# Optimization experiments

Measured on AMD Instinct MI355X. Metric: run time of the kernel, lower is better.

The kernel has to match this reference:

```python
import jax, jax.numpy as jnp
import numpy as np
from jax import lax

WS = 8           # window size
NH = 16          # num heads
BN_EPS = 1e-5


def _rel_pos_index(ws):
    # static Swin relative-position index, shape (ws*ws, ws*ws)
    coords = jnp.stack(jnp.meshgrid(jnp.arange(ws), jnp.arange(ws), indexing='ij'))  # (2,ws,ws)
    cf = coords.reshape(2, -1)                                   # (2, n)
    rel = cf[:, :, None] - cf[:, None, :]                        # (2, n, n)
    return (rel[0] + ws - 1) * (2 * ws - 1) + (rel[1] + ws - 1)  # (n, n)


def setup_inputs() -> dict:
    key = jax.random.key(0)
    ks = jax.random.split(key, 9)
    C = 256
    x = jax.random.normal(ks[0], (2, C, 256, 256), dtype=jnp.float32)
    qkv_w = jax.random.normal(ks[1], (3 * C, C), dtype=jnp.float32) * 0.02
    bias_table = jax.random.normal(ks[2], ((2 * WS - 1) ** 2, NH), dtype=jnp.float32) * 0.02
    dw_w = jax.random.normal(ks[3], (C, 1, 3, 3), dtype=jnp.float32) * 0.1
    bn_gamma = 1.0 + 0.1 * jax.random.normal(ks[4], (C,), dtype=jnp.float32)
    bn_beta = 0.1 * jax.random.normal(ks[5], (C,), dtype=jnp.float32)
    bn_mean = 0.1 * jax.random.normal(ks[6], (C,), dtype=jnp.float32)
    bn_var = jax.random.uniform(ks[7], (C,), dtype=jnp.float32) + 0.5
    pw_w = jax.random.normal(ks[8], (C, C), dtype=jnp.float32) * 0.05
    return {"x": x, "qkv_w": qkv_w, "bias_table": bias_table, "dw_w": dw_w,
            "bn_gamma": bn_gamma, "bn_beta": bn_beta, "bn_mean": bn_mean,
            "bn_var": bn_var, "pw_w": pw_w}


def _lmsa(x, qkv_w, bias_table, dw_w, bn_gamma, bn_beta, bn_mean, bn_var, pw_w):
    B, C, H, W = x.shape
    h, ws = NH, WS
    d = C // h
    scale = d ** (-0.5)
    short = x
    # pad H,W to multiples of ws (reflect); static no-op if already divisible
    pad_h, pad_w = (-H) % ws, (-W) % ws
    if pad_h or pad_w:
        x = jnp.pad(x, ((0, 0), (0, 0), (0, pad_h), (0, pad_w)), mode='reflect')
    Hp, Wp = x.shape[2], x.shape[3]
    hh, ww = Hp // ws, Wp // ws
    # 1x1 conv qkv: C -> 3C
    qkv = jnp.einsum('oc,bchw->bohw', qkv_w, x)
    # window partition: (B,3C,Hp,Wp) -> (3, B*hh*ww, h, ws*ws, d)
    qkv = qkv.reshape(B, 3, h, d, hh, ws, ww, ws)
    qkv = qkv.transpose(1, 0, 4, 6, 2, 5, 7, 3).reshape(3, B * hh * ww, h, ws * ws, d)
    q, k, v = qkv[0], qkv[1], qkv[2]
    dots = jnp.einsum('bhid,bhjd->bhij', q, k) * scale
    # relative position bias
    idx = _rel_pos_index(ws)                       # (n, n)
    bias = bias_table[idx]                         # (n, n, h)
    dots = dots + bias.transpose(2, 0, 1)[None]    # (1, h, n, n)
    attn = jax.nn.softmax(dots, axis=-1)
    out = jnp.einsum('bhij,bhjd->bhid', attn, v)
    # window merge: -> (B, C, Hp, Wp)
    out = out.reshape(B, hh, ww, h, ws, ws, d).transpose(0, 3, 6, 1, 4, 2, 5)
    out = out.reshape(B, C, Hp, Wp)
    out = out[:, :, :H, :W] + short
    # pad_out: reflect pad right/bottom by 1
    out = jnp.pad(out, ((0, 0), (0, 0), (0, 1), (0, 1)), mode='reflect')
    # proj = SeparableConvBN: depthwise3x3 -> BN (inference) -> pointwise1x1
    y = lax.conv_general_dilated(out, dw_w, window_strides=(1, 1),
                                 padding=((1, 1), (1, 1)),
                                 feature_group_count=C,
                                 dimension_numbers=('NCHW', 'OIHW', 'NCHW'))
    inv = bn_gamma / jnp.sqrt(bn_var + BN_EPS)
    y = y * inv[None, :, None, None] + (bn_beta - bn_mean * inv)[None, :, None, None]
    y = jnp.einsum('oc,bchw->bohw', pw_w, y)
    return y[:, :, :H, :W]


def reference(x, qkv_w, bias_table, dw_w, bn_gamma, bn_beta, bn_mean, bn_var, pw_w):
    return _lmsa(x, qkv_w, bias_table, dw_w, bn_gamma, bn_beta, bn_mean, bn_var, pw_w)
```

## Files before the change

kernel.cpp:

```cpp
#include <hip/hip_runtime.h>
#include <hip/hip_bf16.h>

typedef unsigned short us;
typedef unsigned int   u32;
typedef __bf16 bf16_t;
typedef bf16_t bf16x8 __attribute__((ext_vector_type(8)));
typedef float  f32x4  __attribute__((ext_vector_type(4)));
typedef us     usx4   __attribute__((ext_vector_type(4)));
typedef us     usx8   __attribute__((ext_vector_type(8)));

#define HWSZ 65536

__device__ __forceinline__ float b2f(us u) {
    union { u32 i; float f; } t; t.i = ((u32)u) << 16; return t.f;
}
__device__ __forceinline__ us f2b(float f) {
    union { float f; u32 i; } t; t.f = f;
    u32 r = t.i + 0x7fff + ((t.i >> 16) & 1);
    return (us)(r >> 16);
}
__device__ __forceinline__ void gl_lds16(const us* g, us* l) {
    __builtin_amdgcn_global_load_lds(
        (const __attribute__((address_space(1))) u32*)g,
        (__attribute__((address_space(3))) u32*)l, 16, 0, 0);
}

__global__ __launch_bounds__(256) void prep(
        const float* __restrict__ qkv_w, const float* __restrict__ pw_w,
        const float* __restrict__ g, const float* __restrict__ bt,
        const float* __restrict__ mn, const float* __restrict__ vr,
        us* __restrict__ wb, us* __restrict__ pwb, float* __restrict__ ivad) {
    int tid = blockIdx.x * 256 + threadIdx.x;
    if (tid < 768 * 256) wb[tid] = f2b(qkv_w[tid]);
    if (tid < 256 * 256) pwb[tid] = f2b(pw_w[tid]);
    if (tid < 256) {
        float iv = g[tid] / sqrtf(vr[tid] + 1e-5f);
        ivad[tid] = iv;
        ivad[256 + tid] = bt[tid] - mn[tid] * iv;
    }
}

__global__ __launch_bounds__(256) void transpose_x(
        const float* __restrict__ x, us* __restrict__ xt) {
    __shared__ float ls[64][65];
    const int b  = blockIdx.z;
    const int c0 = blockIdx.y * 64;
    const int p0 = blockIdx.x * 64;
    const int tid = threadIdx.x;
    const int tr  = tid >> 4;
    const int tc4 = (tid & 15) << 2;
    const float* xb = x + ((size_t)b * 256 + c0) * HWSZ + p0;
    #pragma unroll
    for (int q = 0; q < 4; ++q) {
        int c = tr + 16 * q;
        float4 v = *(const float4*)&xb[(size_t)c * HWSZ + tc4];
        ls[c][tc4 + 0] = v.x; ls[c][tc4 + 1] = v.y;
        ls[c][tc4 + 2] = v.z; ls[c][tc4 + 3] = v.w;
    }
    __syncthreads();
    #pragma unroll
    for (int q = 0; q < 4; ++q) {
        int pp = tr + 16 * q;
        usx4 o;
        o[0] = f2b(ls[tc4 + 0][pp]); o[1] = f2b(ls[tc4 + 1][pp]);
        o[2] = f2b(ls[tc4 + 2][pp]); o[3] = f2b(ls[tc4 + 3][pp]);
        *(usx4*)&xt[((size_t)b * HWSZ + p0 + pp) * 256 + c0 + tc4] = o;
    }
}

__global__ __launch_bounds__(256) void qkv_mfma(
        const us* __restrict__ xt, const us* __restrict__ wb,
        us* __restrict__ qkv) {
    __shared__ __align__(16) us As[128 * 32];
    __shared__ __align__(16) us Bs[128 * 32];
    const int tid  = threadIdx.x;
    const int wv   = tid >> 6;
    const int lane = tid & 63;
    const int p0 = blockIdx.x * 128;
    const int o0 = blockIdx.y * 128;
    const int b  = blockIdx.z;
    const us* Ab = xt + ((size_t)b * HWSZ + p0) * 256;
    const us* Bb = wb + (size_t)o0 * 256;
    const int lr = lane & 15;
    const int k8 = lane >> 4;
    const int wm = wv >> 1, wn = wv & 1;
    const int srow = lane >> 2;
    const int sch  = (lane & 3) << 3;

    f32x4 acc[4][4];
    #pragma unroll
    for (int i = 0; i < 4; ++i)
        #pragma unroll
        for (int j = 0; j < 4; ++j) acc[i][j] = (f32x4){0.f, 0.f, 0.f, 0.f};

    for (int kt = 0; kt < 8; ++kt) {
        const int c0 = kt * 32;
        #pragma unroll
        for (int i = 0; i < 2; ++i) {
            int rb = 32 * wv + 16 * i;
            gl_lds16(Ab + (size_t)(rb + srow) * 256 + c0 + sch, &As[rb * 32]);
            gl_lds16(Bb + (size_t)(rb + srow) * 256 + c0 + sch, &Bs[rb * 32]);
        }
        __syncthreads();
        bf16x8 af[4], bg[4];
        #pragma unroll
        for (int i = 0; i < 4; ++i)
            af[i] = *(const bf16x8*)&As[(64 * wm + 16 * i + lr) * 32 + k8 * 8];
        #pragma unroll
        for (int j = 0; j < 4; ++j)
            bg[j] = *(const bf16x8*)&Bs[(64 * wn + 16 * j + lr) * 32 + k8 * 8];
        #pragma unroll
        for (int i = 0; i < 4; ++i)
            #pragma unroll
            for (int j = 0; j < 4; ++j)
                acc[i][j] = __builtin_amdgcn_mfma_f32_16x16x32_bf16(
                    af[i], bg[j], acc[i][j], 0, 0, 0);
        __syncthreads();
    }
    #pragma unroll
    for (int i = 0; i < 4; ++i) {
        int pr = p0 + 64 * wm + 16 * i + 4 * k8;
        #pragma unroll
        for (int j = 0; j < 4; ++j) {
            int oc = o0 + 64 * wn + 16 * j + lr;
            #pragma unroll
            for (int rr = 0; rr < 4; ++rr)
                qkv[((size_t)b * HWSZ + pr + rr) * 768 + oc] = f2b(acc[i][j][rr]);
        }
    }
}

__global__ __launch_bounds__(64) void attn_kernel(
        const us* __restrict__ qkv, const us* __restrict__ xt,
        const float* __restrict__ bias_table, us* __restrict__ att) {
    const int bx = blockIdx.x;
    const int head = bx & 15;
    const int w = (bx >> 4) & 1023;
    const int b = bx >> 14;
    const int wy = w >> 5, wx = w & 31;
    const int t = threadIdx.x;
    const int p = (wy * 8 + (t >> 3)) * 256 + wx * 8 + (t & 7);
    const size_t rowb = (size_t)b * HWSZ + p;
    const size_t gq = rowb * 768 + head * 16;

    __shared__ float ks[64][20];
    __shared__ float vs[64][20];
    __shared__ float bias_s[228];

    usx8 k0v = *(const usx8*)&qkv[gq + 256];
    usx8 k1v = *(const usx8*)&qkv[gq + 256 + 8];
    usx8 v0v = *(const usx8*)&qkv[gq + 512];
    usx8 v1v = *(const usx8*)&qkv[gq + 512 + 8];
    #pragma unroll
    for (int d = 0; d < 8; ++d) {
        ks[t][d] = b2f(k0v[d]); ks[t][d + 8] = b2f(k1v[d]);
        vs[t][d] = b2f(v0v[d]); vs[t][d + 8] = b2f(v1v[d]);
    }
    usx8 q0 = *(const usx8*)&qkv[gq];
    usx8 q1 = *(const usx8*)&qkv[gq + 8];
    float qr[16];
    #pragma unroll
    for (int d = 0; d < 8; ++d) {
        qr[d] = b2f(q0[d]) * 0.25f; qr[d + 8] = b2f(q1[d]) * 0.25f;
    }
    #pragma unroll
    for (int r = 0; r < 4; ++r) {
        int idx = r * 64 + t;
        if (idx < 225) bias_s[idx] = bias_table[idx * 16 + head];
    }
    __syncthreads();

    float dots[64];
    #pragma unroll 16
    for (int j = 0; j < 64; ++j) {
        float kk[16];
        *(float4*)&kk[0]  = *(const float4*)&ks[j][0];
        *(float4*)&kk[4]  = *(const float4*)&ks[j][4];
        *(float4*)&kk[8]  = *(const float4*)&ks[j][8];
        *(float4*)&kk[12] = *(const float4*)&ks[j][12];
        float s = 0.f;
        #pragma unroll
        for (int d = 0; d < 16; ++d) s = fmaf(qr[d], kk[d], s);
        dots[j] = s;
    }
    const int iy = t >> 3, ix = t & 7;
    float mx = -1e30f;
    #pragma unroll
    for (int j = 0; j < 64; ++j) {
        int jy = j >> 3, jx = j & 7;
        dots[j] += bias_s[(iy - jy + 7) * 15 + (ix - jx + 7)];
        mx = fmaxf(mx, dots[j]);
    }
    float ssum = 0.f;
    #pragma unroll
    for (int j = 0; j < 64; ++j) {
        float e = __expf(dots[j] - mx);
        dots[j] = e; ssum += e;
    }
    const float sinv = 1.0f / ssum;

    float o[16];
    #pragma unroll
    for (int d = 0; d < 16; ++d) o[d] = 0.f;
    #pragma unroll 16
    for (int j = 0; j < 64; ++j) {
        float vv[16];
        *(float4*)&vv[0]  = *(const float4*)&vs[j][0];
        *(float4*)&vv[4]  = *(const float4*)&vs[j][4];
        *(float4*)&vv[8]  = *(const float4*)&vs[j][8];
        *(float4*)&vv[12] = *(const float4*)&vs[j][12];
        float a = dots[j];
        #pragma unroll
        for (int d = 0; d < 16; ++d) o[d] = fmaf(a, vv[d], o[d]);
    }
    usx8 r0 = *(const usx8*)&xt[rowb * 256 + head * 16];
    usx8 r1 = *(const usx8*)&xt[rowb * 256 + head * 16 + 8];
    usx8 s0, s1;
    #pragma unroll
    for (int d = 0; d < 8; ++d) {
        s0[d] = f2b(o[d] * sinv + b2f(r0[d]));
        s1[d] = f2b(o[d + 8] * sinv + b2f(r1[d]));
    }
    *(usx8*)&att[rowb * 256 + head * 16]     = s0;
    *(usx8*)&att[rowb * 256 + head * 16 + 8] = s1;
}

__global__ __launch_bounds__(256) void dwbn(
        const us* __restrict__ att, const float* __restrict__ dw_w,
        const float* __restrict__ ivad, us* __restrict__ ybn) {
    const int tid = threadIdx.x;
    const int cg = tid & 63;
    const int pl = tid >> 6;
    const int b  = blockIdx.y;
    const int pbase = blockIdx.x * 256;
    const int c4 = cg * 4;
    float w[9][4], iv[4], ad[4];
    #pragma unroll
    for (int cc = 0; cc < 4; ++cc) {
        #pragma unroll
        for (int k = 0; k < 9; ++k) w[k][cc] = dw_w[(c4 + cc) * 9 + k];
        iv[cc] = ivad[c4 + cc];
        ad[cc] = ivad[256 + c4 + cc];
    }
    const us* ab = att + (size_t)b * HWSZ * 256;
    us* yb = ybn + (size_t)b * HWSZ * 256;
    for (int ch = 0; ch < 64; ++ch) {
        const int p = pbase + ch * 4 + pl;
        const int y = p >> 8, x = p & 255;
        float acc[4] = {0.f, 0.f, 0.f, 0.f};
        #pragma unroll
        for (int dy = -1; dy <= 1; ++dy) {
            int yy = y + dy;
            if (yy < 0) continue;
            if (yy > 255) yy = 254;
            #pragma unroll
            for (int dx = -1; dx <= 1; ++dx) {
                int xx = x + dx;
                if (xx < 0) continue;
                if (xx > 255) xx = 254;
                usx4 vv = *(const usx4*)&ab[((size_t)(yy << 8) + xx) * 256 + c4];
                const int k = (dy + 1) * 3 + dx + 1;
                acc[0] = fmaf(w[k][0], b2f(vv[0]), acc[0]);
                acc[1] = fmaf(w[k][1], b2f(vv[1]), acc[1]);
                acc[2] = fmaf(w[k][2], b2f(vv[2]), acc[2]);
                acc[3] = fmaf(w[k][3], b2f(vv[3]), acc[3]);
            }
        }
        usx4 o;
        o[0] = f2b(acc[0] * iv[0] + ad[0]);
        o[1] = f2b(acc[1] * iv[1] + ad[1]);
        o[2] = f2b(acc[2] * iv[2] + ad[2]);
        o[3] = f2b(acc[3] * iv[3] + ad[3]);
        *(usx4*)&yb[(size_t)p * 256 + c4] = o;
    }
}

__global__ __launch_bounds__(256) void pw_mfma(
        const us* __restrict__ ybn, const us* __restrict__ pwb,
        float* __restrict__ out) {
    __shared__ __align__(16) us As[128 * 32];
    __shared__ __align__(16) us Bs[128 * 32];
    const int tid  = threadIdx.x;
    const int wv   = tid >> 6;
    const int lane = tid & 63;
    const int p0 = blockIdx.x * 128;
    const int o0 = blockIdx.y * 128;
    const int b  = blockIdx.z;
    const us* Ab = ybn + ((size_t)b * HWSZ + p0) * 256;
    const us* Bb = pwb + (size_t)o0 * 256;
    const int lr = lane & 15;
    const int k8 = lane >> 4;
    const int wm = wv >> 1, wn = wv & 1;
    const int srow = lane >> 2;
    const int sch  = (lane & 3) << 3;

    f32x4 acc[4][4];
    #pragma unroll
    for (int i = 0; i < 4; ++i)
        #pragma unroll
        for (int j = 0; j < 4; ++j) acc[i][j] = (f32x4){0.f, 0.f, 0.f, 0.f};

    for (int kt = 0; kt < 8; ++kt) {
        const int c0 = kt * 32;
        #pragma unroll
        for (int i = 0; i < 2; ++i) {
            int rb = 32 * wv + 16 * i;
            gl_lds16(Ab + (size_t)(rb + srow) * 256 + c0 + sch, &As[rb * 32]);
            gl_lds16(Bb + (size_t)(rb + srow) * 256 + c0 + sch, &Bs[rb * 32]);
        }
        __syncthreads();
        bf16x8 af[4], bg[4];
        #pragma unroll
        for (int i = 0; i < 4; ++i)
            af[i] = *(const bf16x8*)&As[(64 * wm + 16 * i + lr) * 32 + k8 * 8];
        #pragma unroll
        for (int j = 0; j < 4; ++j)
            bg[j] = *(const bf16x8*)&Bs[(64 * wn + 16 * j + lr) * 32 + k8 * 8];
        #pragma unroll
        for (int i = 0; i < 4; ++i)
            #pragma unroll
            for (int j = 0; j < 4; ++j)
                acc[i][j] = __builtin_amdgcn_mfma_f32_16x16x32_bf16(
                    af[i], bg[j], acc[i][j], 0, 0, 0);
        __syncthreads();
    }
    #pragma unroll
    for (int i = 0; i < 4; ++i) {
        int pr = p0 + 64 * wm + 16 * i + 4 * k8;
        #pragma unroll
        for (int j = 0; j < 4; ++j) {
            int oc = o0 + 64 * wn + 16 * j + lr;
            *(f32x4*)&out[((size_t)b * 256 + oc) * HWSZ + pr] = acc[i][j];
        }
    }
}

extern "C" void kernel_launch(void* const* d_in, const int* in_sizes, int n_in,
                              void* d_out, int out_size, void* d_ws, size_t ws_size,
                              hipStream_t stream) {
    const float* x          = (const float*)d_in[0];
    const float* qkv_w      = (const float*)d_in[1];
    const float* bias_table = (const float*)d_in[2];
    const float* dw_w       = (const float*)d_in[3];
    const float* bn_gamma   = (const float*)d_in[4];
    const float* bn_beta    = (const float*)d_in[5];
    const float* bn_mean    = (const float*)d_in[6];
    const float* bn_var     = (const float*)d_in[7];
    const float* pw_w       = (const float*)d_in[8];
    float* out = (float*)d_out;

    char* ws = (char*)d_ws;
    us*    xt   = (us*)ws;
    us*    qkv  = (us*)(ws + 67108864);
    us*    att  = (us*)(ws + 268435456);
    us*    wb   = (us*)(ws + 335544320);
    us*    pwb  = (us*)(ws + 335937536);
    float* ivad = (float*)(ws + 336068608);
    us*    ybn  = xt;

    prep<<<768, 256, 0, stream>>>(qkv_w, pw_w, bn_gamma, bn_beta, bn_mean,
                                  bn_var, wb, pwb, ivad);
    transpose_x<<<dim3(1024, 4, 2), 256, 0, stream>>>(x, xt);
    qkv_mfma<<<dim3(512, 6, 2), 256, 0, stream>>>(xt, wb, qkv);
    attn_kernel<<<2 * 1024 * 16, 64, 0, stream>>>(qkv, xt, bias_table, att);
    dwbn<<<dim3(256, 2), 256, 0, stream>>>(att, dw_w, ivad, ybn);
    pw_mfma<<<dim3(512, 2, 2), 256, 0, stream>>>(ybn, pwb, out);
}
```

Baseline: 1.131 ms.

## Restructure attention per window, vectorize qkv stores and depthwise conv loads

Attention now runs one 256-thread block per window that handles all 16 heads, staging K/V for eight heads at a time in LDS as bf16 via direct global-to-LDS loads, replacing 64-thread per-head blocks. The q scale is folded into the qkv weights during prep. The qkv GEMM swaps its MFMA operands so each lane writes four contiguous output channels as one vector store. The depthwise conv handles 8 channels per thread with 16-byte loads. Together these aim to cut launch count, uncoalesced stores and narrow memory accesses, at the cost of a larger LDS footprint and more register pressure in the attention kernel.

```diff
diff --git a/kernel.cpp b/kernel.cpp
--- a/kernel.cpp
+++ b/kernel.cpp
@@ -31,7 +31,12 @@
         const float* __restrict__ mn, const float* __restrict__ vr,
         us* __restrict__ wb, us* __restrict__ pwb, float* __restrict__ ivad) {
     int tid = blockIdx.x * 256 + threadIdx.x;
-    if (tid < 768 * 256) wb[tid] = f2b(qkv_w[tid]);
+    if (tid < 768 * 256) {
+        int o = tid >> 8;
+        float v = qkv_w[tid];
+        if (o < 256) v *= 0.25f;
+        wb[tid] = f2b(v);
+    }
     if (tid < 256 * 256) pwb[tid] = f2b(pw_w[tid]);
     if (tid < 256) {
         float iv = g[tid] / sqrtf(vr[tid] + 1e-5f);
@@ -114,140 +119,147 @@
             #pragma unroll
             for (int j = 0; j < 4; ++j)
                 acc[i][j] = __builtin_amdgcn_mfma_f32_16x16x32_bf16(
-                    af[i], bg[j], acc[i][j], 0, 0, 0);
+                    bg[j], af[i], acc[i][j], 0, 0, 0);
         __syncthreads();
     }
     #pragma unroll
     for (int i = 0; i < 4; ++i) {
-        int pr = p0 + 64 * wm + 16 * i + 4 * k8;
+        int pr = p0 + 64 * wm + 16 * i + lr;
         #pragma unroll
         for (int j = 0; j < 4; ++j) {
-            int oc = o0 + 64 * wn + 16 * j + lr;
-            #pragma unroll
-            for (int rr = 0; rr < 4; ++rr)
-                qkv[((size_t)b * HWSZ + pr + rr) * 768 + oc] = f2b(acc[i][j][rr]);
-        }
-    }
-}
-
-__global__ __launch_bounds__(64) void attn_kernel(
+            int oc = o0 + 64 * wn + 16 * j + 4 * k8;
+            usx4 t;
+            #pragma unroll
+            for (int rr = 0; rr < 4; ++rr) t[rr] = f2b(acc[i][j][rr]);
+            *(usx4*)&qkv[((size_t)b * HWSZ + pr) * 768 + oc] = t;
+        }
+    }
+}
+
+__global__ __launch_bounds__(256) void attn_kernel(
         const us* __restrict__ qkv, const us* __restrict__ xt,
         const float* __restrict__ bias_table, us* __restrict__ att) {
-    const int bx = blockIdx.x;
-    const int head = bx & 15;
-    const int w = (bx >> 4) & 1023;
-    const int b = bx >> 14;
+    const int w  = blockIdx.x & 1023;
+    const int b  = blockIdx.x >> 10;
     const int wy = w >> 5, wx = w & 31;
-    const int t = threadIdx.x;
-    const int p = (wy * 8 + (t >> 3)) * 256 + wx * 8 + (t & 7);
-    const size_t rowb = (size_t)b * HWSZ + p;
-    const size_t gq = rowb * 768 + head * 16;
-
-    __shared__ float ks[64][20];
-    __shared__ float vs[64][20];
-    __shared__ float bias_s[228];
-
-    usx8 k0v = *(const usx8*)&qkv[gq + 256];
-    usx8 k1v = *(const usx8*)&qkv[gq + 256 + 8];
-    usx8 v0v = *(const usx8*)&qkv[gq + 512];
-    usx8 v1v = *(const usx8*)&qkv[gq + 512 + 8];
-    #pragma unroll
-    for (int d = 0; d < 8; ++d) {
-        ks[t][d] = b2f(k0v[d]); ks[t][d + 8] = b2f(k1v[d]);
-        vs[t][d] = b2f(v0v[d]); vs[t][d + 8] = b2f(v1v[d]);
-    }
-    usx8 q0 = *(const usx8*)&qkv[gq];
-    usx8 q1 = *(const usx8*)&qkv[gq + 8];
-    float qr[16];
-    #pragma unroll
-    for (int d = 0; d < 8; ++d) {
-        qr[d] = b2f(q0[d]) * 0.25f; qr[d + 8] = b2f(q1[d]) * 0.25f;
-    }
-    #pragma unroll
-    for (int r = 0; r < 4; ++r) {
-        int idx = r * 64 + t;
-        if (idx < 225) bias_s[idx] = bias_table[idx * 16 + head];
-    }
-    __syncthreads();
-
-    float dots[64];
-    #pragma unroll 16
-    for (int j = 0; j < 64; ++j) {
-        float kk[16];
-        *(float4*)&kk[0]  = *(const float4*)&ks[j][0];
-        *(float4*)&kk[4]  = *(const float4*)&ks[j][4];
-        *(float4*)&kk[8]  = *(const float4*)&ks[j][8];
-        *(float4*)&kk[12] = *(const float4*)&ks[j][12];
-        float s = 0.f;
-        #pragma unroll
-        for (int d = 0; d < 16; ++d) s = fmaf(qr[d], kk[d], s);
-        dots[j] = s;
-    }
-    const int iy = t >> 3, ix = t & 7;
-    float mx = -1e30f;
-    #pragma unroll
-    for (int j = 0; j < 64; ++j) {
-        int jy = j >> 3, jx = j & 7;
-        dots[j] += bias_s[(iy - jy + 7) * 15 + (ix - jx + 7)];
-        mx = fmaxf(mx, dots[j]);
-    }
-    float ssum = 0.f;
-    #pragma unroll
-    for (int j = 0; j < 64; ++j) {
-        float e = __expf(dots[j] - mx);
-        dots[j] = e; ssum += e;
-    }
-    const float sinv = 1.0f / ssum;
-
-    float o[16];
-    #pragma unroll
-    for (int d = 0; d < 16; ++d) o[d] = 0.f;
-    #pragma unroll 16
-    for (int j = 0; j < 64; ++j) {
-        float vv[16];
-        *(float4*)&vv[0]  = *(const float4*)&vs[j][0];
-        *(float4*)&vv[4]  = *(const float4*)&vs[j][4];
-        *(float4*)&vv[8]  = *(const float4*)&vs[j][8];
-        *(float4*)&vv[12] = *(const float4*)&vs[j][12];
-        float a = dots[j];
-        #pragma unroll
-        for (int d = 0; d < 16; ++d) o[d] = fmaf(a, vv[d], o[d]);
-    }
-    usx8 r0 = *(const usx8*)&xt[rowb * 256 + head * 16];
-    usx8 r1 = *(const usx8*)&xt[rowb * 256 + head * 16 + 8];
-    usx8 s0, s1;
-    #pragma unroll
-    for (int d = 0; d < 8; ++d) {
-        s0[d] = f2b(o[d] * sinv + b2f(r0[d]));
-        s1[d] = f2b(o[d + 8] * sinv + b2f(r1[d]));
-    }
-    *(usx8*)&att[rowb * 256 + head * 16]     = s0;
-    *(usx8*)&att[rowb * 256 + head * 16 + 8] = s1;
+    const int tid  = threadIdx.x;
+    const int wave = tid >> 6;
+    const int lane = tid & 63;
+
+    __shared__ __align__(16) us kv8[64][256];
+    __shared__ float bias_s[16][225];
+
+    const int p_lane = (wy * 8 + (lane >> 3)) * 256 + wx * 8 + (lane & 7);
+    const size_t rowb = (size_t)b * HWSZ + p_lane;
+    const int iy = lane >> 3, ix = lane & 7;
+
+    const int tt  = lane >> 5;
+    const int seg = (lane >> 4) & 1;
+    const int co  = (lane & 15) << 3;
+
+    for (int n = tid; n < 3600; n += 256)
+        bias_s[n & 15][n >> 4] = bias_table[n];
+
+    #pragma unroll 1
+    for (int hb = 0; hb < 2; ++hb) {
+        #pragma unroll
+        for (int i = 0; i < 8; ++i) {
+            int t0 = wave * 16 + 2 * i;
+            int t  = t0 + tt;
+            int pt = (wy * 8 + (t >> 3)) * 256 + wx * 8 + (t & 7);
+            const us* src = qkv + ((size_t)b * HWSZ + pt) * 768
+                            + 256 + seg * 256 + hb * 128 + co;
+            gl_lds16(src, &kv8[t0][0]);
+        }
+        __syncthreads();
+
+        #pragma unroll 1
+        for (int hh = 0; hh < 2; ++hh) {
+            const int h  = hb * 8 + wave * 2 + hh;
+            const int hc = (wave * 2 + hh) << 4;
+            const size_t gq = rowb * 768 + h * 16;
+            usx8 q0 = *(const usx8*)&qkv[gq];
+            usx8 q1 = *(const usx8*)&qkv[gq + 8];
+            float qr[16];
+            #pragma unroll
+            for (int d = 0; d < 8; ++d) {
+                qr[d] = b2f(q0[d]); qr[d + 8] = b2f(q1[d]);
+            }
+            float dots[64];
+            #pragma unroll
+            for (int j = 0; j < 64; ++j) {
+                usx8 k0 = *(const usx8*)&kv8[j][hc];
+                usx8 k1 = *(const usx8*)&kv8[j][hc + 8];
+                float s = 0.f;
+                #pragma unroll
+                for (int d = 0; d < 8; ++d) s = fmaf(qr[d], b2f(k0[d]), s);
+                #pragma unroll
+                for (int d = 0; d < 8; ++d) s = fmaf(qr[d + 8], b2f(k1[d]), s);
+                dots[j] = s;
+            }
+            float mx = -1e30f;
+            #pragma unroll
+            for (int j = 0; j < 64; ++j) {
+                dots[j] += bias_s[h][(iy - (j >> 3) + 7) * 15 + (ix - (j & 7) + 7)];
+                mx = fmaxf(mx, dots[j]);
+            }
+            float ssum = 0.f;
+            #pragma unroll
+            for (int j = 0; j < 64; ++j) {
+                float e = __expf(dots[j] - mx);
+                dots[j] = e; ssum += e;
+            }
+            const float sinv = 1.0f / ssum;
+            float o[16];
+            #pragma unroll
+            for (int d = 0; d < 16; ++d) o[d] = 0.f;
+            #pragma unroll
+            for (int j = 0; j < 64; ++j) {
+                usx8 v0 = *(const usx8*)&kv8[j][128 + hc];
+                usx8 v1 = *(const usx8*)&kv8[j][128 + hc + 8];
+                float a = dots[j];
+                #pragma unroll
+                for (int d = 0; d < 8; ++d) o[d]     = fmaf(a, b2f(v0[d]), o[d]);
+                #pragma unroll
+                for (int d = 0; d < 8; ++d) o[d + 8] = fmaf(a, b2f(v1[d]), o[d + 8]);
+            }
+            usx8 r0 = *(const usx8*)&xt[rowb * 256 + h * 16];
+            usx8 r1 = *(const usx8*)&xt[rowb * 256 + h * 16 + 8];
+            usx8 s0, s1;
+            #pragma unroll
+            for (int d = 0; d < 8; ++d) {
+                s0[d] = f2b(o[d] * sinv + b2f(r0[d]));
+                s1[d] = f2b(o[d + 8] * sinv + b2f(r1[d]));
+            }
+            *(usx8*)&att[rowb * 256 + h * 16]     = s0;
+            *(usx8*)&att[rowb * 256 + h * 16 + 8] = s1;
+        }
+        if (hb == 0) __syncthreads();
+    }
 }
 
 __global__ __launch_bounds__(256) void dwbn(
         const us* __restrict__ att, const float* __restrict__ dw_w,
         const float* __restrict__ ivad, us* __restrict__ ybn) {
     const int tid = threadIdx.x;
-    const int cg = tid & 63;
-    const int pl = tid >> 6;
+    const int c8 = (tid & 31) * 8;
+    const int pl = tid >> 5;
     const int b  = blockIdx.y;
     const int pbase = blockIdx.x * 256;
-    const int c4 = cg * 4;
-    float w[9][4], iv[4], ad[4];
-    #pragma unroll
-    for (int cc = 0; cc < 4; ++cc) {
-        #pragma unroll
-        for (int k = 0; k < 9; ++k) w[k][cc] = dw_w[(c4 + cc) * 9 + k];
-        iv[cc] = ivad[c4 + cc];
-        ad[cc] = ivad[256 + c4 + cc];
+    float w[9][8], iv[8], ad[8];
+    #pragma unroll
+    for (int cc = 0; cc < 8; ++cc) {
+        #pragma unroll
+        for (int k = 0; k < 9; ++k) w[k][cc] = dw_w[(c8 + cc) * 9 + k];
+        iv[cc] = ivad[c8 + cc];
+        ad[cc] = ivad[256 + c8 + cc];
     }
     const us* ab = att + (size_t)b * HWSZ * 256;
     us* yb = ybn + (size_t)b * HWSZ * 256;
-    for (int ch = 0; ch < 64; ++ch) {
-        const int p = pbase + ch * 4 + pl;
+    for (int it = 0; it < 32; ++it) {
+        const int p = pbase + it * 8 + pl;
         const int y = p >> 8, x = p & 255;
-        float acc[4] = {0.f, 0.f, 0.f, 0.f};
+        float acc[8] = {0.f, 0.f, 0.f, 0.f, 0.f, 0.f, 0.f, 0.f};
         #pragma unroll
         for (int dy = -1; dy <= 1; ++dy) {
             int yy = y + dy;
@@ -258,20 +270,17 @@
                 int xx = x + dx;
                 if (xx < 0) continue;
                 if (xx > 255) xx = 254;
-                usx4 vv = *(const usx4*)&ab[((size_t)(yy << 8) + xx) * 256 + c4];
+                usx8 vv = *(const usx8*)&ab[((size_t)(yy << 8) + xx) * 256 + c8];
                 const int k = (dy + 1) * 3 + dx + 1;
-                acc[0] = fmaf(w[k][0], b2f(vv[0]), acc[0]);
-                acc[1] = fmaf(w[k][1], b2f(vv[1]), acc[1]);
-                acc[2] = fmaf(w[k][2], b2f(vv[2]), acc[2]);
-                acc[3] = fmaf(w[k][3], b2f(vv[3]), acc[3]);
-            }
-        }
-        usx4 o;
-        o[0] = f2b(acc[0] * iv[0] + ad[0]);
-        o[1] = f2b(acc[1] * iv[1] + ad[1]);
-        o[2] = f2b(acc[2] * iv[2] + ad[2]);
-        o[3] = f2b(acc[3] * iv[3] + ad[3]);
-        *(usx4*)&yb[(size_t)p * 256 + c4] = o;
+                #pragma unroll
+                for (int cc = 0; cc < 8; ++cc)
+                    acc[cc] = fmaf(w[k][cc], b2f(vv[cc]), acc[cc]);
+            }
+        }
+        usx8 o;
+        #pragma unroll
+        for (int cc = 0; cc < 8; ++cc) o[cc] = f2b(acc[cc] * iv[cc] + ad[cc]);
+        *(usx8*)&yb[(size_t)p * 256 + c8] = o;
     }
 }
 
@@ -362,7 +371,7 @@
                                   bn_var, wb, pwb, ivad);
     transpose_x<<<dim3(1024, 4, 2), 256, 0, stream>>>(x, xt);
     qkv_mfma<<<dim3(512, 6, 2), 256, 0, stream>>>(xt, wb, qkv);
-    attn_kernel<<<2 * 1024 * 16, 64, 0, stream>>>(qkv, xt, bias_table, att);
+    attn_kernel<<<2048, 256, 0, stream>>>(qkv, xt, bias_table, att);
     dwbn<<<dim3(256, 2), 256, 0, stream>>>(att, dw_w, ivad, ybn);
     pw_mfma<<<dim3(512, 2, 2), 256, 0, stream>>>(ybn, pwb, out);
 }
```

Result: faster. 985.4 us (-12.9%).
